# Performance work log

Hardware: AMD Instinct MI355X
Metric: run time of the kernel (lower is better)

Reference implementation:

```python
import jax, jax.numpy as jnp
import numpy as np

N = 2_000_000
IN_CH = 10
OUT_HALF = 32  # out_channel // 2 since last_layer=False
V = 50_000


def _bn(x, gamma, beta, eps):
    # BatchNorm1d in training mode: batch stats, biased variance
    m = jnp.mean(x, axis=0)
    v = jnp.var(x, axis=0)
    return (x - m) * jax.lax.rsqrt(v + eps) * gamma + beta


def _finite_or_zero(x):
    # torch_scatter fills empty segments with 0; jax segment_min/max give +/-inf
    return jnp.where(jnp.isfinite(x), x, 0.0)


def setup_inputs() -> dict:
    key = jax.random.key(0)
    ks = jax.random.split(key, 12)
    s = lambda *sh: 0.05
    inp = {
        "inputs": jax.random.normal(ks[0], (N, IN_CH), dtype=jnp.float32),
        "unq_inv": jax.random.randint(ks[1], (N,), 0, V, dtype=jnp.int32),
        "num_segments": V,
        # self.linear: in_channel -> out_half
        "W_lin": jax.random.normal(ks[2], (IN_CH, OUT_HALF), jnp.float32) * 0.3,
        "b_lin": jnp.zeros((OUT_HALF,), jnp.float32),
        # self.norm (BN, eps=1e-3)
        "g_norm": jnp.ones((OUT_HALF,), jnp.float32),
        "be_norm": jnp.zeros((OUT_HALF,), jnp.float32),
        # self.w = Linear -> BN -> ReLU -> Linear(->1)
        "W_w1": jax.random.normal(ks[3], (IN_CH, OUT_HALF), jnp.float32) * 0.3,
        "b_w1": jnp.zeros((OUT_HALF,), jnp.float32),
        "g_wbn": jnp.ones((OUT_HALF,), jnp.float32),
        "be_wbn": jnp.zeros((OUT_HALF,), jnp.float32),
        "W_w2": jax.random.normal(ks[4], (OUT_HALF, 1), jnp.float32) * 0.3,
        "b_w2": jnp.zeros((1,), jnp.float32),
        # ChannelAttn: fc1 out_half -> 2*out_half, fc2 -> out_half
        "W_fc1": jax.random.normal(ks[5], (OUT_HALF, 2 * OUT_HALF), jnp.float32) * 0.2,
        "b_fc1": jnp.zeros((2 * OUT_HALF,), jnp.float32),
        "W_fc2": jax.random.normal(ks[6], (2 * OUT_HALF, OUT_HALF), jnp.float32) * 0.2,
        "b_fc2": jnp.zeros((OUT_HALF,), jnp.float32),
    }
    return inp


def reference(inputs, unq_inv, num_segments, W_lin, b_lin, g_norm, be_norm,
              W_w1, b_w1, g_wbn, be_wbn, W_w2, b_w2,
              W_fc1, b_fc1, W_fc2, b_fc2):
    V_ = num_segments
    v = inputs @ W_lin + b_lin                      # [N, C]
    norm_v = _bn(v, g_norm, be_norm, 1e-3)
    x = jax.nn.relu(norm_v)                         # [N, C]

    # scatter_max over pillars
    q_max = _finite_or_zero(jax.ops.segment_max(x, unq_inv, num_segments=V_))  # [V, C]

    # weight branch: Linear -> BN -> ReLU -> Linear(1), then scatter_softmax
    h = jax.nn.relu(_bn(inputs @ W_w1 + b_w1, g_wbn, be_wbn, 1e-5))
    weight = h @ W_w2 + b_w2                        # [N, 1]
    w_max = jax.ops.segment_max(weight, unq_inv, num_segments=V_)
    w_max = _finite_or_zero(w_max)
    e = jnp.exp(weight - w_max[unq_inv])            # [N, 1]
    denom = jax.ops.segment_sum(e, unq_inv, num_segments=V_)
    soft_weight = e / jnp.maximum(denom, 1e-16)[unq_inv]

    # scatter_mean(soft_weight * v)
    sw_v = soft_weight * v                          # [N, C]
    seg_sum = jax.ops.segment_sum(sw_v, unq_inv, num_segments=V_)
    cnt = jax.ops.segment_sum(jnp.ones((inputs.shape[0], 1), v.dtype), unq_inv, num_segments=V_)
    weight_x = seg_sum / jnp.maximum(cnt, 1.0)      # [V, C]

    # channel attention from scatter_min of norm_v
    min_feat = _finite_or_zero(jax.ops.segment_min(norm_v, unq_inv, num_segments=V_))
    cw = jax.nn.sigmoid(jax.nn.relu(min_feat @ W_fc1 + b_fc1) @ W_fc2 + b_fc2)  # [V, C]

    final_feat = cw * q_max + (1.0 - cw) * weight_x  # [V, C]
    return jnp.concatenate([x, final_feat[unq_inv]], axis=-1)  # [N, 2C]
```

## Files before the change

### kernel.cpp

```cpp
#include <hip/hip_runtime.h>
#include <math.h>

#define VSEG 50000
#define CH 32
#define KIN 10
#define NB_STATS 512
#define STATS_B 256
#define SCAN_B 256
#define NBLK_SCAN ((VSEG + SCAN_B - 1) / SCAN_B)
#define SEGS_PER_BLOCK 4

__global__ __launch_bounds__(256) void init_cnt_k(unsigned* cnt) {
    int i = blockIdx.x * blockDim.x + threadIdx.x;
    if (i < VSEG) cnt[i] = 0u;
}

__global__ __launch_bounds__(STATS_B) void stats_partial_k(const float* __restrict__ in,
                                                           const int* __restrict__ idx, int n,
                                                           float* __restrict__ partial,
                                                           unsigned* __restrict__ cnt,
                                                           unsigned* __restrict__ rank) {
    float acc[65];
#pragma unroll
    for (int q = 0; q < 65; ++q) acc[q] = 0.0f;

    for (int i = blockIdx.x * blockDim.x + threadIdx.x; i < n; i += gridDim.x * blockDim.x) {
        const float* ip = in + (size_t)i * KIN;
        float x[KIN];
#pragma unroll
        for (int k = 0; k < KIN; ++k) x[k] = ip[k];
#pragma unroll
        for (int k = 0; k < KIN; ++k) acc[k] += x[k];
#pragma unroll
        for (int k = 0; k < KIN; ++k) {
#pragma unroll
            for (int l = k; l < KIN; ++l)
                acc[10 + k * (21 - k) / 2 + (l - k)] += x[k] * x[l];
        }
        rank[i] = atomicAdd(&cnt[idx[i]], 1u);
    }

    __shared__ float red[STATS_B / 64][65];
    int lane = threadIdx.x & 63, wid = threadIdx.x >> 6;
#pragma unroll
    for (int q = 0; q < 65; ++q) {
        float v = acc[q];
#pragma unroll
        for (int off = 32; off > 0; off >>= 1) v += __shfl_down(v, off, 64);
        if (lane == 0) red[wid][q] = v;
    }
    __syncthreads();
    if (threadIdx.x < 65) {
        float s = 0.0f;
#pragma unroll
        for (int w = 0; w < STATS_B / 64; ++w) s += red[w][threadIdx.x];
        partial[blockIdx.x * 65 + threadIdx.x] = s;
    }
}

__global__ __launch_bounds__(128) void stats_finalize_k(
    const float* __restrict__ partial, int nb, int n,
    const float* __restrict__ Wlin, const float* __restrict__ blin,
    const float* __restrict__ g1, const float* __restrict__ be1,
    const float* __restrict__ Ww1, const float* __restrict__ bw1,
    const float* __restrict__ g2, const float* __restrict__ be2,
    float* __restrict__ ss) {
    __shared__ double tot[65];
    int t = threadIdx.x;
    if (t < 65) {
        double s = 0.0;
        for (int b = 0; b < nb; ++b) s += (double)partial[b * 65 + t];
        tot[t] = s;
    }
    __syncthreads();
    if (t < 64) {
        int c = t & 31;
        const float* W = (t < 32) ? Wlin : Ww1;
        double bb = (double)((t < 32) ? blin[c] : bw1[c]);
        double g  = (double)((t < 32) ? g1[c] : g2[c]);
        double be = (double)((t < 32) ? be1[c] : be2[c]);
        double eps = (t < 32) ? 1e-3 : 1e-5;
        double invN = 1.0 / (double)n;
        double m0 = 0.0;
        for (int k = 0; k < KIN; ++k) m0 += tot[k] * (double)W[k * CH + c];
        m0 *= invN;
        double q0 = 0.0;
        for (int k = 0; k < KIN; ++k)
            for (int l = k; l < KIN; ++l) {
                int qi = 10 + k * (21 - k) / 2 + (l - k);
                double coef = (k == l) ? 1.0 : 2.0;
                q0 += coef * tot[qi] * (double)W[k * CH + c] * (double)W[l * CH + c];
            }
        q0 *= invN;
        double var = q0 - m0 * m0;
        double mean = m0 + bb;
        double sc = g / sqrt(var + eps);
        float scale = (float)sc;
        float shift = (float)(be - mean * sc);
        if (t < 32) { ss[c] = scale; ss[32 + c] = shift; }
        else        { ss[64 + c] = scale; ss[96 + c] = shift; }
    }
}

__global__ __launch_bounds__(256) void scan1_k(const unsigned* __restrict__ cnt,
                                               unsigned* __restrict__ segstart,
                                               unsigned* __restrict__ bsum) {
    int t = threadIdx.x;
    int i = blockIdx.x * SCAN_B + t;
    unsigned v = (i < VSEG) ? cnt[i] : 0u;
    int lane = t & 63, w = t >> 6;
    unsigned incl = v;
#pragma unroll
    for (int off = 1; off < 64; off <<= 1) {
        unsigned s = __shfl_up(incl, off, 64);
        if (lane >= off) incl += s;
    }
    __shared__ unsigned wsum[4];
    if (lane == 63) wsum[w] = incl;
    __syncthreads();
    unsigned wo = 0;
#pragma unroll
    for (int k = 0; k < 4; ++k) wo += (k < w) ? wsum[k] : 0u;
    if (i < VSEG) segstart[i] = wo + incl - v;
    if (t == SCAN_B - 1) bsum[blockIdx.x] = wo + incl;
}

__global__ __launch_bounds__(256) void scan2_k(unsigned* __restrict__ bsum, int nb) {
    int t = threadIdx.x;
    unsigned v = (t < nb) ? bsum[t] : 0u;
    int lane = t & 63, w = t >> 6;
    unsigned incl = v;
#pragma unroll
    for (int off = 1; off < 64; off <<= 1) {
        unsigned s = __shfl_up(incl, off, 64);
        if (lane >= off) incl += s;
    }
    __shared__ unsigned wsum[4];
    if (lane == 63) wsum[w] = incl;
    __syncthreads();
    unsigned wo = 0;
#pragma unroll
    for (int k = 0; k < 4; ++k) wo += (k < w) ? wsum[k] : 0u;
    if (t < nb) bsum[t] = wo + incl - v;
}

__global__ __launch_bounds__(256) void scan3_k(unsigned* __restrict__ segstart,
                                               const unsigned* __restrict__ bsum) {
    int i = blockIdx.x * SCAN_B + threadIdx.x;
    if (i < VSEG) segstart[i] += bsum[blockIdx.x];
}

__global__ __launch_bounds__(256) void scatterW_k(
    const float* __restrict__ in, const int* __restrict__ idx, int n,
    const float* __restrict__ Ww1, const float* __restrict__ bw1,
    const float* __restrict__ Ww2, const float* __restrict__ bw2,
    const float* __restrict__ ss,
    const unsigned* __restrict__ segstart, const unsigned* __restrict__ rank,
    int* __restrict__ sortedIdx, float* __restrict__ wsorted) {
    __shared__ float sWw1[KIN * CH], sbw1[CH], sWw2[CH], sssU[64];
    __shared__ float sbw2;
    for (int i = threadIdx.x; i < KIN * CH; i += blockDim.x) sWw1[i] = Ww1[i];
    for (int i = threadIdx.x; i < CH; i += blockDim.x) { sbw1[i] = bw1[i]; sWw2[i] = Ww2[i]; }
    for (int i = threadIdx.x; i < 64; i += blockDim.x) sssU[i] = ss[64 + i];
    if (threadIdx.x == 0) sbw2 = bw2[0];
    __syncthreads();

    int i = blockIdx.x * blockDim.x + threadIdx.x;
    if (i >= n) return;

    const float* ip = in + (size_t)i * KIN;
    float x[KIN];
#pragma unroll
    for (int k = 0; k < KIN; ++k) x[k] = ip[k];

    float w = sbw2;
#pragma unroll 4
    for (int c = 0; c < CH; ++c) {
        float u = sbw1[c];
#pragma unroll
        for (int k = 0; k < KIN; ++k) u = fmaf(x[k], sWw1[k * CH + c], u);
        float hu = fmaxf(fmaf(u, sssU[c], sssU[32 + c]), 0.0f);
        w = fmaf(hu, sWw2[c], w);
    }

    unsigned p = segstart[idx[i]] + rank[i];
    sortedIdx[p] = i;
    wsorted[p] = w;
}

__global__ __launch_bounds__(256) void mega_k(
    const float* __restrict__ in, const int* __restrict__ sortedIdx,
    const float* __restrict__ wsorted,
    const unsigned* __restrict__ segstart, const unsigned* __restrict__ cnt,
    const float* __restrict__ Wlin, const float* __restrict__ blin,
    const float* __restrict__ ss,
    const float* __restrict__ Wfc1, const float* __restrict__ bfc1,
    const float* __restrict__ Wfc2, const float* __restrict__ bfc2,
    float* __restrict__ out) {
    __shared__ float sWlin[KIN * CH], sblin[CH], sssV[64];
    __shared__ float sW1[CH * 64], sb1[64], sW2[64 * CH], sb2[CH];
    __shared__ float qmL[SEGS_PER_BLOCK][CH], mnL[SEGS_PER_BLOCK][CH];
    __shared__ float SL[SEGS_PER_BLOCK][CH], dL[SEGS_PER_BLOCK];
    __shared__ float a1L[SEGS_PER_BLOCK][64], ffL[SEGS_PER_BLOCK][CH];
    __shared__ int mS[SEGS_PER_BLOCK];

    for (int i = threadIdx.x; i < KIN * CH; i += blockDim.x) sWlin[i] = Wlin[i];
    for (int i = threadIdx.x; i < CH; i += blockDim.x) { sblin[i] = blin[i]; sb2[i] = bfc2[i]; }
    for (int i = threadIdx.x; i < 64; i += blockDim.x) { sssV[i] = ss[i]; sb1[i] = bfc1[i]; }
    for (int i = threadIdx.x; i < CH * 64; i += blockDim.x) { sW1[i] = Wfc1[i]; sW2[i] = Wfc2[i]; }
    __syncthreads();

    int lane = threadIdx.x & 63, wid = threadIdx.x >> 6;
    int c = lane & 31, h = lane >> 5;
    int seg = blockIdx.x * SEGS_PER_BLOCK + wid;

    int m = 0; unsigned base = 0;
    if (seg < VSEG) { m = (int)cnt[seg]; base = segstart[seg]; }
    if (lane == 0) mS[wid] = m;

    float scale = sssV[c], shift = sssV[32 + c], bl = sblin[c];
    float qm = 0.0f, mn = INFINITY, d = 0.0f, S = 0.0f;

    for (int p = h; p < m; p += 2) {
        int pi = sortedIdx[base + p];
        const float* ip = in + (size_t)pi * KIN;
        float v = bl;
#pragma unroll
        for (int k = 0; k < KIN; ++k) v = fmaf(ip[k], sWlin[k * CH + c], v);
        float nv = fmaf(v, scale, shift);
        float x  = fmaxf(nv, 0.0f);
        out[(size_t)pi * 64 + c] = x;
        float e = __expf(wsorted[base + p]);
        qm = fmaxf(qm, x);
        mn = fminf(mn, nv);
        d += e;
        S = fmaf(e, v, S);
    }
    qm = fmaxf(qm, __shfl_xor(qm, 32));
    mn = fminf(mn, __shfl_xor(mn, 32));
    d += __shfl_xor(d, 32);
    S += __shfl_xor(S, 32);
    if (h == 0) {
        qmL[wid][c] = qm;
        mnL[wid][c] = (m > 0) ? mn : 0.0f;
        SL[wid][c]  = S;
    }
    if (lane == 0) dL[wid] = d;
    __syncthreads();

    {
        int sl = threadIdx.x >> 6, j = threadIdx.x & 63;
        float a = sb1[j];
#pragma unroll 8
        for (int cc = 0; cc < CH; ++cc) a = fmaf(mnL[sl][cc], sW1[cc * 64 + j], a);
        a1L[sl][j] = fmaxf(a, 0.0f);
    }
    __syncthreads();

    if (threadIdx.x < SEGS_PER_BLOCK * CH) {
        int sl = threadIdx.x >> 5, cc = threadIdx.x & 31;
        float z = sb2[cc];
#pragma unroll 8
        for (int j = 0; j < 64; ++j) z = fmaf(a1L[sl][j], sW2[j * CH + cc], z);
        float cw = 1.0f / (1.0f + __expf(-z));
        float dn = fmaxf(dL[sl], 1e-16f);
        float ct = fmaxf((float)mS[sl], 1.0f);
        float wx = SL[sl][cc] / (dn * ct);
        ffL[sl][cc] = cw * qmL[sl][cc] + (1.0f - cw) * wx;
    }
    __syncthreads();

    float ff = ffL[wid][c];
    for (int p = h; p < m; p += 2) {
        int pi = sortedIdx[base + p];
        out[(size_t)pi * 64 + 32 + c] = ff;
    }
}

extern "C" void kernel_launch(void* const* d_in, const int* in_sizes, int n_in,
                              void* d_out, int out_size, void* d_ws, size_t ws_size,
                              hipStream_t stream) {
    const float* inputs = (const float*)d_in[0];
    const int*   unq    = (const int*)d_in[1];
    const float* Wlin = (const float*)d_in[3];
    const float* blin = (const float*)d_in[4];
    const float* g1   = (const float*)d_in[5];
    const float* be1  = (const float*)d_in[6];
    const float* Ww1  = (const float*)d_in[7];
    const float* bw1  = (const float*)d_in[8];
    const float* g2   = (const float*)d_in[9];
    const float* be2  = (const float*)d_in[10];
    const float* Ww2  = (const float*)d_in[11];
    const float* bw2  = (const float*)d_in[12];
    const float* Wfc1 = (const float*)d_in[13];
    const float* bfc1 = (const float*)d_in[14];
    const float* Wfc2 = (const float*)d_in[15];
    const float* bfc2 = (const float*)d_in[16];

    const int N = in_sizes[0] / KIN;
    float* out = (float*)d_out;

    char* ws = (char*)d_ws;
    size_t off = 0;
    auto alloc = [&](size_t bytes) -> void* {
        void* p = ws + off;
        off += (bytes + 255) & ~(size_t)255;
        return p;
    };
    unsigned* cnt      = (unsigned*)alloc((size_t)VSEG * 4);
    unsigned* segstart = (unsigned*)alloc((size_t)VSEG * 4);
    unsigned* bsum     = (unsigned*)alloc((size_t)NBLK_SCAN * 4);
    float*    ssbuf    = (float*)   alloc(128 * 4);
    float*    partial  = (float*)   alloc((size_t)NB_STATS * 65 * 4);
    unsigned* rank     = (unsigned*)alloc((size_t)N * 4);
    int*      sortedIdx= (int*)     alloc((size_t)N * 4);
    float*    wsorted  = (float*)   alloc((size_t)N * 4);

    const int B = 256;
    int g_pt   = (N + B - 1) / B;
    int g_seg  = (VSEG + B - 1) / B;
    int g_mega = (VSEG + SEGS_PER_BLOCK - 1) / SEGS_PER_BLOCK;

    init_cnt_k<<<g_seg, B, 0, stream>>>(cnt);
    stats_partial_k<<<NB_STATS, STATS_B, 0, stream>>>(inputs, unq, N, partial, cnt, rank);
    stats_finalize_k<<<1, 128, 0, stream>>>(partial, NB_STATS, N,
                                            Wlin, blin, g1, be1, Ww1, bw1, g2, be2, ssbuf);
    scan1_k<<<NBLK_SCAN, SCAN_B, 0, stream>>>(cnt, segstart, bsum);
    scan2_k<<<1, SCAN_B, 0, stream>>>(bsum, NBLK_SCAN);
    scan3_k<<<NBLK_SCAN, SCAN_B, 0, stream>>>(segstart, bsum);
    scatterW_k<<<g_pt, B, 0, stream>>>(inputs, unq, N, Ww1, bw1, Ww2, bw2, ssbuf,
                                       segstart, rank, sortedIdx, wsorted);
    mega_k<<<g_mega, B, 0, stream>>>(inputs, sortedIdx, wsorted, segstart, cnt,
                                     Wlin, blin, ssbuf, Wfc1, bfc1, Wfc2, bfc2, out);
}
```

Before: 631.0 us.

## Pack sorted index and weight into int2, split segment halves contiguously, unroll gathers by four

Stores the sorted point index and its softmax logit together as one int2, so the scatter kernel issues a single 8-byte store and the segment kernel a single load per point. Each half-wave now takes a contiguous half of the segment instead of alternating points. The main loop is unrolled by four so four independent input-row gathers are in flight at once, hiding gather latency. The cost is more registers per thread and a remainder loop.

```diff
diff --git a/kernel.cpp b/kernel.cpp
--- a/kernel.cpp
+++ b/kernel.cpp
@@ -156,7 +156,7 @@
     const float* __restrict__ Ww2, const float* __restrict__ bw2,
     const float* __restrict__ ss,
     const unsigned* __restrict__ segstart, const unsigned* __restrict__ rank,
-    int* __restrict__ sortedIdx, float* __restrict__ wsorted) {
+    int2* __restrict__ pw) {
     __shared__ float sWw1[KIN * CH], sbw1[CH], sWw2[CH], sssU[64];
     __shared__ float sbw2;
     for (int i = threadIdx.x; i < KIN * CH; i += blockDim.x) sWw1[i] = Ww1[i];
@@ -184,13 +184,11 @@
     }
 
     unsigned p = segstart[idx[i]] + rank[i];
-    sortedIdx[p] = i;
-    wsorted[p] = w;
+    pw[p] = make_int2(i, __float_as_int(w));
 }
 
 __global__ __launch_bounds__(256) void mega_k(
-    const float* __restrict__ in, const int* __restrict__ sortedIdx,
-    const float* __restrict__ wsorted,
+    const float* __restrict__ in, const int2* __restrict__ pw,
     const unsigned* __restrict__ segstart, const unsigned* __restrict__ cnt,
     const float* __restrict__ Wlin, const float* __restrict__ blin,
     const float* __restrict__ ss,
@@ -218,24 +216,65 @@
     if (seg < VSEG) { m = (int)cnt[seg]; base = segstart[seg]; }
     if (lane == 0) mS[wid] = m;
 
+    int mh = (m + 1) >> 1;
+    int ps = h ? mh : 0;
+    int pe = h ? m : mh;
+
     float scale = sssV[c], shift = sssV[32 + c], bl = sblin[c];
     float qm = 0.0f, mn = INFINITY, d = 0.0f, S = 0.0f;
 
-    for (int p = h; p < m; p += 2) {
-        int pi = sortedIdx[base + p];
-        const float* ip = in + (size_t)pi * KIN;
-        float v = bl;
-#pragma unroll
-        for (int k = 0; k < KIN; ++k) v = fmaf(ip[k], sWlin[k * CH + c], v);
-        float nv = fmaf(v, scale, shift);
-        float x  = fmaxf(nv, 0.0f);
-        out[(size_t)pi * 64 + c] = x;
-        float e = __expf(wsorted[base + p]);
-        qm = fmaxf(qm, x);
-        mn = fminf(mn, nv);
-        d += e;
-        S = fmaf(e, v, S);
-    }
+    int p = ps;
+    for (; p + 3 < pe; p += 4) {
+        int2 q0 = pw[base + p], q1 = pw[base + p + 1];
+        int2 q2 = pw[base + p + 2], q3 = pw[base + p + 3];
+        const float* ip0 = in + (size_t)q0.x * KIN;
+        const float* ip1 = in + (size_t)q1.x * KIN;
+        const float* ip2 = in + (size_t)q2.x * KIN;
+        const float* ip3 = in + (size_t)q3.x * KIN;
+        float r0[KIN], r1[KIN], r2[KIN], r3[KIN];
+#pragma unroll
+        for (int k = 0; k < KIN; ++k) { r0[k] = ip0[k]; r1[k] = ip1[k]; r2[k] = ip2[k]; r3[k] = ip3[k]; }
+        float v0 = bl, v1 = bl, v2 = bl, v3 = bl;
+#pragma unroll
+        for (int k = 0; k < KIN; ++k) {
+            float wk = sWlin[k * CH + c];
+            v0 = fmaf(r0[k], wk, v0);
+            v1 = fmaf(r1[k], wk, v1);
+            v2 = fmaf(r2[k], wk, v2);
+            v3 = fmaf(r3[k], wk, v3);
+        }
+        float nv0 = fmaf(v0, scale, shift), nv1 = fmaf(v1, scale, shift);
+        float nv2 = fmaf(v2, scale, shift), nv3 = fmaf(v3, scale, shift);
+        float x0 = fmaxf(nv0, 0.0f), x1 = fmaxf(nv1, 0.0f);
+        float x2 = fmaxf(nv2, 0.0f), x3 = fmaxf(nv3, 0.0f);
+        out[(size_t)q0.x * 64 + c] = x0;
+        out[(size_t)q1.x * 64 + c] = x1;
+        out[(size_t)q2.x * 64 + c] = x2;
+        out[(size_t)q3.x * 64 + c] = x3;
+        float e0 = __expf(__int_as_float(q0.y)), e1 = __expf(__int_as_float(q1.y));
+        float e2 = __expf(__int_as_float(q2.y)), e3 = __expf(__int_as_float(q3.y));
+        qm = fmaxf(fmaxf(fmaxf(qm, x0), fmaxf(x1, x2)), x3);
+        mn = fminf(fminf(fminf(mn, nv0), fminf(nv1, nv2)), nv3);
+        d += (e0 + e1) + (e2 + e3);
+        S = fmaf(e0, v0, S); S = fmaf(e1, v1, S);
+        S = fmaf(e2, v2, S); S = fmaf(e3, v3, S);
+    }
+    for (; p < pe; ++p) {
+        int2 q0 = pw[base + p];
+        const float* ip0 = in + (size_t)q0.x * KIN;
+        float v0 = bl;
+#pragma unroll
+        for (int k = 0; k < KIN; ++k) v0 = fmaf(ip0[k], sWlin[k * CH + c], v0);
+        float nv0 = fmaf(v0, scale, shift);
+        float x0 = fmaxf(nv0, 0.0f);
+        out[(size_t)q0.x * 64 + c] = x0;
+        float e0 = __expf(__int_as_float(q0.y));
+        qm = fmaxf(qm, x0);
+        mn = fminf(mn, nv0);
+        d += e0;
+        S = fmaf(e0, v0, S);
+    }
+
     qm = fmaxf(qm, __shfl_xor(qm, 32));
     mn = fminf(mn, __shfl_xor(mn, 32));
     d += __shfl_xor(d, 32);
@@ -271,8 +310,8 @@
     __syncthreads();
 
     float ff = ffL[wid][c];
-    for (int p = h; p < m; p += 2) {
-        int pi = sortedIdx[base + p];
+    for (p = ps; p < pe; ++p) {
+        int pi = pw[base + p].x;
         out[(size_t)pi * 64 + 32 + c] = ff;
     }
 }
@@ -313,8 +352,7 @@
     float*    ssbuf    = (float*)   alloc(128 * 4);
     float*    partial  = (float*)   alloc((size_t)NB_STATS * 65 * 4);
     unsigned* rank     = (unsigned*)alloc((size_t)N * 4);
-    int*      sortedIdx= (int*)     alloc((size_t)N * 4);
-    float*    wsorted  = (float*)   alloc((size_t)N * 4);
+    int2*     pw       = (int2*)    alloc((size_t)N * 8);
 
     const int B = 256;
     int g_pt   = (N + B - 1) / B;
@@ -329,7 +367,7 @@
     scan2_k<<<1, SCAN_B, 0, stream>>>(bsum, NBLK_SCAN);
     scan3_k<<<NBLK_SCAN, SCAN_B, 0, stream>>>(segstart, bsum);
     scatterW_k<<<g_pt, B, 0, stream>>>(inputs, unq, N, Ww1, bw1, Ww2, bw2, ssbuf,
-                                       segstart, rank, sortedIdx, wsorted);
-    mega_k<<<g_mega, B, 0, stream>>>(inputs, sortedIdx, wsorted, segstart, cnt,
+                                       segstart, rank, pw);
+    mega_k<<<g_mega, B, 0, stream>>>(inputs, pw, segstart, cnt,
                                      Wlin, blin, ssbuf, Wfc1, bfc1, Wfc2, bfc2, out);
 }
```

Measured after the change: 527.6 us (median of 2 runs). 1.2x faster.
